# Kernel tuning notes

Hardware: AMD Instinct MI355X
Metric: run time of the kernel (lower is better)

The kernel has to match this reference:

```python
import jax, jax.numpy as jnp
import numpy as np
from jax.scipy.special import gammaln, xlogy

H, K, V = 8, 64, 192          # heads, key_size, value_size
F = 192                        # num_relative_position_features
LN2 = 0.6931471805599453


def positional_features(T):
    """Enformer positional basis: exp half-life, central mask, gamma pdf;
    non-symmetric -> concat [emb, sign(pos)*emb]. Returns [2T-1, F]."""
    n = F // 6                                  # basis per class per symmetry
    pos = jnp.arange(-(T - 1), T, dtype=jnp.float32)   # [2T-1]
    ap = jnp.abs(pos)[:, None]                  # [2T-1, 1]
    # exponential (min_half_life=3.0, seq_length=T)
    max_range = jnp.log(float(T)) / LN2
    half_life = 2.0 ** jnp.linspace(3.0, max_range, n)
    fe = jnp.exp(-LN2 / half_life * ap)
    # central mask
    widths = 2.0 ** jnp.arange(1, n + 1, dtype=jnp.float32) - 1.0
    fm = (widths > ap).astype(jnp.float32)
    # gamma (stddev=T/(2n), start_mean=T/n)
    stddev = T / (2.0 * n)
    mean = jnp.linspace(T / float(n), float(T), n)
    conc = (mean / stddev) ** 2
    rate = mean / stddev ** 2
    log_p = xlogy(conc - 1.0, ap) - rate * ap - (gammaln(conc) - conc * jnp.log(rate))
    prob = jnp.exp(log_p) + 1e-8
    fg = prob / jnp.max(prob)
    emb = jnp.concatenate([fe, fm, fg], axis=-1)               # [2T-1, F/2]
    emb = jnp.concatenate([emb, jnp.sign(pos)[:, None] * emb], axis=-1)  # [2T-1, F]
    return emb


def relative_shift(x):
    """TransformerXL relative shift. x: [B,H,T,2T-1] -> [B,H,T,T]."""
    b, h, t1, r = x.shape                       # r == 2*t1 - 1
    x = jnp.pad(x, ((0, 0), (0, 0), (0, 0), (1, 0)))  # [B,H,T,2T]
    x = x.reshape(b, h, r + 1, t1)[:, :, 1:, :]        # [B,H,2T-1,T]
    x = x.reshape(b, h, t1, r)
    return x[..., :t1]


def setup_inputs() -> dict:
    key = jax.random.key(0)
    ks = jax.random.split(key, 8)
    B, T, D = 2, 1536, 1536
    s = 0.02
    return {
        "x": jax.random.normal(ks[0], (B, T, D), jnp.float32),
        "Wq": jax.random.normal(ks[1], (D, H * K), jnp.float32) * s,
        "Wk": jax.random.normal(ks[2], (D, H * K), jnp.float32) * s,
        "Wv": jax.random.normal(ks[3], (D, H * V), jnp.float32) * s,
        "Wrk": jax.random.normal(ks[4], (F, H * K), jnp.float32) * s,
        "Wemb": jax.random.normal(ks[5], (H * V, D), jnp.float32) * s,
        "r_w_bias": jax.random.normal(ks[6], (1, H, 1, K), jnp.float32) * s,
        "r_r_bias": jax.random.normal(ks[7], (1, H, 1, K), jnp.float32) * s,
    }


def reference(x, Wq, Wk, Wv, Wrk, Wemb, r_w_bias, r_r_bias):
    B, T, D = x.shape
    q = (x @ Wq).reshape(B, T, H, K).transpose(0, 2, 1, 3)   # [B,H,T,K]
    k = (x @ Wk).reshape(B, T, H, K).transpose(0, 2, 1, 3)
    v = (x @ Wv).reshape(B, T, H, V).transpose(0, 2, 1, 3)   # [B,H,T,V]
    q = q * (K ** -0.5)                                       # scaling
    emb = positional_features(T)                              # [2T-1, F]
    r_k = (emb @ Wrk).reshape(2 * T - 1, H, K).transpose(1, 0, 2)  # [H,2T-1,K]
    content = jnp.einsum('bhqk,bhmk->bhqm', q + r_w_bias, k)       # [B,H,T,T]
    rel = jnp.einsum('bhqk,hmk->bhqm', q + r_r_bias, r_k)          # [B,H,T,2T-1]
    logits = content + relative_shift(rel)
    w = jax.nn.softmax(logits, axis=-1)
    out = jnp.einsum('bhqm,bhmv->bhqv', w, v)                      # [B,H,T,V]
    out = out.transpose(0, 2, 1, 3).reshape(B, T, H * V)
    return out @ Wemb
```

## Files before the change

kernel.cpp:

```cpp
#include <hip/hip_runtime.h>
#include <stdint.h>

#define DEVI __device__ __forceinline__
#define LOG2E 1.4426950408889634f

typedef short bf16x8 __attribute__((ext_vector_type(8)));
typedef float f32x4 __attribute__((ext_vector_type(4)));

#define PMAX 0.01867013f

DEVI float b2f(unsigned short u) {
  union { unsigned u32; float f; } x;
  x.u32 = ((unsigned)u) << 16;
  return x.f;
}
DEVI unsigned short f2b(float f) {
  union { float f32; unsigned u32; } x;
  x.f32 = f;
  unsigned u = x.u32;
  return (unsigned short)((u + 0x7FFFu + ((u >> 16) & 1u)) >> 16);
}

DEVI void gload16(const unsigned short* g, unsigned short* l) {
  __builtin_amdgcn_global_load_lds(
      (const __attribute__((address_space(1))) void*)g,
      (__attribute__((address_space(3))) void*)l, 16, 0, 0);
}

DEVI float gamma_prob(float ap, int i) {
  float mean = 48.f * (float)(i + 1);
  float conc = (mean / 24.f) * (mean / 24.f);
  float rate = mean / 576.f;
  if (ap == 0.f) return 1e-8f;
  float logp = (conc - 1.f) * logf(ap) - rate * ap - (lgammaf(conc) - conc * logf(rate));
  return expf(logp) + 1e-8f;
}

DEVI void dev_transpose(const float* srcf, const unsigned short* srcb, int src_ld,
                        unsigned short* dst, int dst_ld, int rows, int cols,
                        int bx, int by, unsigned short (*t)[33]) {
  int tx = threadIdx.x & 31, ty = threadIdx.x >> 5;
  int r0 = by * 32, c0 = bx * 32;
#pragma unroll
  for (int i = 0; i < 4; i++) {
    int r = r0 + ty + i * 8, cc = c0 + tx;
    if (r < rows && cc < cols)
      t[ty + i * 8][tx] = srcf ? f2b(srcf[(size_t)r * src_ld + cc])
                               : srcb[(size_t)r * src_ld + cc];
  }
  __syncthreads();
#pragma unroll
  for (int i = 0; i < 4; i++) {
    int dr = c0 + ty + i * 8, dc = r0 + tx;
    if (dr < cols && dc < rows) dst[(size_t)dr * dst_ld + dc] = t[tx][ty + i * 8];
  }
}

__global__ __launch_bounds__(256) void k_prep(
    const float* __restrict__ x, const float* __restrict__ Wq,
    const float* __restrict__ Wk, const float* __restrict__ Wv,
    const float* __restrict__ Wemb, const float* __restrict__ Wrk,
    unsigned short* __restrict__ xb, unsigned short* __restrict__ WqkvT,
    unsigned short* __restrict__ WembT, unsigned short* __restrict__ WrkT,
    unsigned short* __restrict__ emb) {
  __shared__ unsigned short t[32][33];
  int bid = blockIdx.x;
  if (bid < 4608) {
    int i = (bid * 256 + threadIdx.x) * 4;
    float4 v = *(const float4*)(x + i);
    ushort4 o;
    o.x = f2b(v.x); o.y = f2b(v.y); o.z = f2b(v.z); o.w = f2b(v.w);
    *(ushort4*)(xb + i) = o;
  } else if (bid < 5376) {
    int s = bid - 4608;
    dev_transpose(Wq, nullptr, 512, WqkvT, 1536, 1536, 512, s % 16, s / 16, t);
  } else if (bid < 6144) {
    int s = bid - 5376;
    dev_transpose(Wk, nullptr, 512, WqkvT + (size_t)512 * 1536, 1536, 1536, 512, s % 16, s / 16, t);
  } else if (bid < 8448) {
    int s = bid - 6144;
    dev_transpose(Wv, nullptr, 1536, WqkvT + (size_t)1024 * 1536, 1536, 1536, 1536, s % 48, s / 48, t);
  } else if (bid < 10752) {
    int s = bid - 8448;
    dev_transpose(Wemb, nullptr, 1536, WembT, 1536, 1536, 1536, s % 48, s / 48, t);
  } else if (bid < 10848) {
    int s = bid - 10752;
    dev_transpose(Wrk, nullptr, 512, WrkT, 192, 192, 512, s % 16, s / 16, t);
  } else {
    int idx = (bid - 10848) * 256 + threadIdx.x;
    if (idx < 3071 * 96) {
      int m = idx / 96, cc = idx % 96;
      float ap = fabsf((float)(m - 1535));
      float val;
      if (cc < 32) {
        float max_range = logf(1536.f) * 1.4426950408889634f;
        float l = 3.f + (float)cc * (max_range - 3.f) / 31.f;
        val = exp2f(-ap * exp2f(-l));
      } else if (cc < 64) {
        float width = exp2f((float)(cc - 31)) - 1.f;
        val = (width > ap) ? 1.f : 0.f;
      } else {
        val = gamma_prob(ap, cc - 64) / PMAX;
      }
      float sgn = (m > 1535) ? 1.f : ((m < 1535) ? -1.f : 0.f);
      emb[(size_t)m * 192 + cc] = f2b(val);
      emb[(size_t)m * 192 + 96 + cc] = f2b(sgn * val);
    }
  }
}

DEVI void dev_gemm(const unsigned short* __restrict__ A, const unsigned short* __restrict__ Bt,
                   unsigned short* Cb, float* Cf, int M, int N, int K,
                   int bx, int by, unsigned short* As, unsigned short* Bs) {
  int tid = threadIdx.x;
  int w = tid >> 6, L = tid & 63, g = L >> 4, c = L & 15;
  int m0 = by << 7, n0 = bx << 7;
  int wm = (w >> 1) << 6, wn = (w & 1) << 6;
  f32x4 acc[4][4];
#pragma unroll
  for (int i = 0; i < 4; i++)
#pragma unroll
    for (int j = 0; j < 4; j++) acc[i][j] = (f32x4){0.f, 0.f, 0.f, 0.f};
  int nkt = K >> 5;
  for (int kt = 0; kt < nkt; kt++) {
    int k0 = kt << 5;
#pragma unroll
    for (int i2 = 0; i2 < 2; i2++) {
      int cidx = tid + (i2 << 8);
      int row = cidx >> 2, kc = (cidx & 3) << 3;
      int ra = m0 + row;
      if (ra >= M) ra = M - 1;
      gload16(A + (size_t)ra * K + k0 + kc, As + cidx * 8);
      gload16(Bt + (size_t)(n0 + row) * K + k0 + kc, Bs + cidx * 8);
    }
    __syncthreads();
    bf16x8 af[4], bfr[4];
#pragma unroll
    for (int t = 0; t < 4; t++) af[t] = *(const bf16x8*)(As + (wm + t * 16 + c) * 32 + g * 8);
#pragma unroll
    for (int t = 0; t < 4; t++) bfr[t] = *(const bf16x8*)(Bs + (wn + t * 16 + c) * 32 + g * 8);
#pragma unroll
    for (int mt = 0; mt < 4; mt++)
#pragma unroll
      for (int nt = 0; nt < 4; nt++)
        acc[mt][nt] = __builtin_amdgcn_mfma_f32_16x16x32_bf16(af[mt], bfr[nt], acc[mt][nt], 0, 0, 0);
    __syncthreads();
  }
#pragma unroll
  for (int mt = 0; mt < 4; mt++)
#pragma unroll
    for (int nt = 0; nt < 4; nt++)
#pragma unroll
      for (int r = 0; r < 4; r++) {
        int rr = m0 + wm + mt * 16 + g * 4 + r;
        if (rr < M) {
          size_t o = (size_t)rr * N + n0 + wn + nt * 16 + c;
          if (Cf) Cf[o] = acc[mt][nt][r];
          else Cb[o] = f2b(acc[mt][nt][r]);
        }
      }
}

__global__ __launch_bounds__(256) void k_gemm(
    const unsigned short* __restrict__ A, const unsigned short* __restrict__ Bt,
    unsigned short* Cb, float* Cf, int M, int N, int K) {
  __shared__ unsigned short sm[8192];
  dev_gemm(A, Bt, Cb, Cf, M, N, K, blockIdx.x, blockIdx.y, sm, sm + 4096);
}

__global__ __launch_bounds__(256) void k_mid(
    const unsigned short* __restrict__ emb, const unsigned short* __restrict__ WrkT,
    unsigned short* __restrict__ rkb, const unsigned short* __restrict__ QKV,
    unsigned short* __restrict__ Vt) {
  __shared__ unsigned short sm[8192];
  int bid = blockIdx.x;
  if (bid < 96) {
    dev_gemm(emb, WrkT, rkb, nullptr, 3071, 512, 192, bid & 3, bid >> 2, sm, sm + 4096);
  } else {
    int tt = bid - 96;
    int which = tt / 2304;
    tt %= 2304;
    dev_transpose(nullptr, QKV + 1024 + (size_t)which * 1536 * 2560, 2560,
                  Vt + (size_t)which * 1536 * 1536, 1536, 1536, 1536,
                  tt % 48, tt / 48, (unsigned short (*)[33])sm);
  }
}

__global__ __launch_bounds__(256, 2) void k_attn(
    const unsigned short* __restrict__ QKV, const unsigned short* __restrict__ rk,
    const unsigned short* __restrict__ Vt, const float* __restrict__ rwb,
    const float* __restrict__ rrb, unsigned short* __restrict__ Opart,
    float* __restrict__ lpart) {
  __shared__ unsigned short lds[24576];
  const int tid = threadIdx.x;
  const int w = tid >> 6, L = tid & 63, g = L >> 4, c = L & 15;
  const int bid = blockIdx.x;
  const int h = bid & 7, b = (bid >> 3) & 1, kh = (bid >> 4) & 3;
  const int i0b = (bid >> 6) << 7;
  const int qp = i0b + w * 32;
  const int bh = b * 8 + h;
  const int c7s = (c & 7) << 3;

  const int lrow8 = L >> 3;
  const int lbo = (((L & 7) * 16) ^ ((lrow8 & 7) << 4));

  bf16x8 aqw[2][2], aqr[2][2];
#pragma unroll
  for (int qi = 0; qi < 2; qi++) {
    const unsigned short* qrow =
        QKV + (size_t)(b * 1536 + qp + qi * 16 + c) * 2560 + h * 64;
#pragma unroll
    for (int ks = 0; ks < 2; ks++) {
      union { bf16x8 v; unsigned short s[8]; } uw, ur;
#pragma unroll
      for (int j = 0; j < 8; j++) {
        int d = ks * 32 + g * 8 + j;
        float qv = b2f(qrow[d]) * 0.125f;
        uw.s[j] = f2b((qv + rwb[h * 64 + d]) * LOG2E);
        ur.s[j] = f2b((qv + rrb[h * 64 + d]) * LOG2E);
      }
      aqw[qi][ks] = uw.v;
      aqr[qi][ks] = ur.v;
    }
  }

  int baddr[4], bsel[4];
#pragma unroll
  for (int r = 0; r < 4; r++) {
    int u = c - (g * 4 + r) + 15;
    baddr[r] = (((g << 4) | (u & 15)) << 2);
    bsel[r] = (u >> 4) & 1;
  }

  f32x4 Ofr[8][3];
#pragma unroll
  for (int s = 0; s < 8; s++)
#pragma unroll
    for (int t = 0; t < 3; t++) Ofr[s][t] = (f32x4){0.f, 0.f, 0.f, 0.f};
  float lrow[2][4] = {{0.f, 0.f, 0.f, 0.f}, {0.f, 0.f, 0.f, 0.f}};

  const unsigned short* rkh = rk + h * 64;
  const size_t kgbase = (size_t)(b * 1536 + kh * 384) * 2560 + 512 + h * 64;
  const size_t vgbase = (size_t)(bh * 192) * 1536 + kh * 384;

  auto stageK = [&](int kt) {
#pragma unroll
    for (int i = 0; i < 2; i++) {
      int key = w * 16 + i * 8 + lrow8;
      const unsigned short* src =
          QKV + kgbase + (size_t)(kt * 64 + key) * 2560 + (lbo >> 1);
      gload16(src, lds + w * 1024 + i * 512);
    }
  };
  auto stageV = [&](int kt) {
#pragma unroll
    for (int i = 0; i < 6; i++) {
      int vd = w * 48 + i * 8 + lrow8;
      const unsigned short* src =
          Vt + vgbase + (size_t)vd * 1536 + kt * 64 + (lbo >> 1);
      gload16(src, lds + 4096 + w * 3072 + i * 512);
    }
  };

  stageK(0);
  __syncthreads();

  for (int jt = 0; jt < 6; jt++) {
    stageV(jt);

    const int j0g = kh * 384 + jt * 64;
    const int moff1 = j0g - (qp + 16) + 1520;

    f32x4 Sc[2][4];
#pragma unroll
    for (int nt = 0; nt < 4; nt++) {
      const int kro = (nt * 16 + c) * 64;
      bf16x8 kf0 = *(const bf16x8*)(lds + kro + ((g * 8) ^ c7s));
      bf16x8 kf1 = *(const bf16x8*)(lds + kro + ((32 + g * 8) ^ c7s));
      f32x4 z0 = (f32x4){0.f, 0.f, 0.f, 0.f};
      z0 = __builtin_amdgcn_mfma_f32_16x16x32_bf16(aqw[0][0], kf0, z0, 0, 0, 0);
      z0 = __builtin_amdgcn_mfma_f32_16x16x32_bf16(aqw[0][1], kf1, z0, 0, 0, 0);
      Sc[0][nt] = z0;
      f32x4 z1 = (f32x4){0.f, 0.f, 0.f, 0.f};
      z1 = __builtin_amdgcn_mfma_f32_16x16x32_bf16(aqw[1][0], kf0, z1, 0, 0, 0);
      z1 = __builtin_amdgcn_mfma_f32_16x16x32_bf16(aqw[1][1], kf1, z1, 0, 0, 0);
      Sc[1][nt] = z1;
    }

    float bandp0[4], bandp1[4];
    {
      int mg = moff1 + c;
      const unsigned short* rrow = rkh + (size_t)mg * 512;
      f32x4 z = (f32x4){0.f, 0.f, 0.f, 0.f};
      z = __builtin_amdgcn_mfma_f32_16x16x32_bf16(aqr[1][0], *(const bf16x8*)(rrow + g * 8), z, 0, 0, 0);
      z = __builtin_amdgcn_mfma_f32_16x16x32_bf16(aqr[1][1], *(const bf16x8*)(rrow + 32 + g * 8), z, 0, 0, 0);
#pragma unroll
      for (int r = 0; r < 4; r++)
        bandp1[r] = __int_as_float(__builtin_amdgcn_ds_bpermute(baddr[r], __float_as_int(z[r])));
    }
#pragma unroll
    for (int j = 1; j <= 5; j++) {
      int mg = moff1 + 16 * j + c;
      if (mg > 3070) mg = 3070;
      const unsigned short* rrow = rkh + (size_t)mg * 512;
      bf16x8 rf0 = *(const bf16x8*)(rrow + g * 8);
      bf16x8 rf1 = *(const bf16x8*)(rrow + 32 + g * 8);
      {
        f32x4 z = (f32x4){0.f, 0.f, 0.f, 0.f};
        z = __builtin_amdgcn_mfma_f32_16x16x32_bf16(aqr[0][0], rf0, z, 0, 0, 0);
        z = __builtin_amdgcn_mfma_f32_16x16x32_bf16(aqr[0][1], rf1, z, 0, 0, 0);
        if (j == 1) {
#pragma unroll
          for (int r = 0; r < 4; r++)
            bandp0[r] = __int_as_float(__builtin_amdgcn_ds_bpermute(baddr[r], __float_as_int(z[r])));
        } else {
          const int nt = j - 2;
#pragma unroll
          for (int r = 0; r < 4; r++) {
            float bandc = __int_as_float(__builtin_amdgcn_ds_bpermute(baddr[r], __float_as_int(z[r])));
            Sc[0][nt][r] += bsel[r] ? bandc : bandp0[r];
            bandp0[r] = bandc;
          }
        }
      }
      if (j <= 4) {
        f32x4 z = (f32x4){0.f, 0.f, 0.f, 0.f};
        z = __builtin_amdgcn_mfma_f32_16x16x32_bf16(aqr[1][0], rf0, z, 0, 0, 0);
        z = __builtin_amdgcn_mfma_f32_16x16x32_bf16(aqr[1][1], rf1, z, 0, 0, 0);
        const int nt = j - 1;
#pragma unroll
        for (int r = 0; r < 4; r++) {
          float bandc = __int_as_float(__builtin_amdgcn_ds_bpermute(baddr[r], __float_as_int(z[r])));
          Sc[1][nt][r] += bsel[r] ? bandc : bandp1[r];
          bandp1[r] = bandc;
        }
      }
    }

#pragma unroll
    for (int qi = 0; qi < 2; qi++) {
      unsigned short* slab = lds + 16384 + (2 * w + qi) * 1024;
#pragma unroll
      for (int nt = 0; nt < 4; nt++)
#pragma unroll
        for (int r = 0; r < 4; r++) {
          float p = exp2f(Sc[qi][nt][r]);
          lrow[qi][r] += p;
          int q = g * 4 + r;
          slab[q * 64 + ((nt * 16 + c) ^ ((q & 7) << 3))] = f2b(p);
        }
    }

    __syncthreads();

    if (jt < 5) stageK(jt + 1);

    bf16x8 vf0[3], vf1[3];
#pragma unroll
    for (int vt = 0; vt < 3; vt++) {
      const int vro = 4096 + (w * 48 + vt * 16 + c) * 64;
      vf0[vt] = *(const bf16x8*)(lds + vro + ((g * 8) ^ c7s));
      vf1[vt] = *(const bf16x8*)(lds + vro + ((32 + g * 8) ^ c7s));
    }
    __builtin_amdgcn_s_setprio(1);
#pragma unroll
    for (int s = 0; s < 8; s++) {
      const unsigned short* slab = lds + 16384 + s * 1024;
      bf16x8 ap0 = *(const bf16x8*)(slab + c * 64 + ((g * 8) ^ c7s));
      bf16x8 ap1 = *(const bf16x8*)(slab + c * 64 + ((32 + g * 8) ^ c7s));
#pragma unroll
      for (int vt = 0; vt < 3; vt++) {
        Ofr[s][vt] = __builtin_amdgcn_mfma_f32_16x16x32_bf16(ap0, vf0[vt], Ofr[s][vt], 0, 0, 0);
        Ofr[s][vt] = __builtin_amdgcn_mfma_f32_16x16x32_bf16(ap1, vf1[vt], Ofr[s][vt], 0, 0, 0);
      }
    }
    __builtin_amdgcn_s_setprio(0);

    __syncthreads();
  }

#pragma unroll
  for (int qi = 0; qi < 2; qi++)
#pragma unroll
    for (int r = 0; r < 4; r++) {
      float s = lrow[qi][r];
      s += __shfl_xor(s, 1, 64);
      s += __shfl_xor(s, 2, 64);
      s += __shfl_xor(s, 4, 64);
      s += __shfl_xor(s, 8, 64);
      lrow[qi][r] = s;
    }
  if (c == 0) {
#pragma unroll
    for (int qi = 0; qi < 2; qi++)
#pragma unroll
      for (int r = 0; r < 4; r++)
        lpart[(size_t)((kh * 2 + b) * 8 + h) * 1536 + qp + qi * 16 + g * 4 + r] =
            lrow[qi][r];
  }
#pragma unroll
  for (int s = 0; s < 8; s++)
#pragma unroll
    for (int vt = 0; vt < 3; vt++)
#pragma unroll
      for (int r = 0; r < 4; r++)
        Opart[(size_t)(kh * 3072 + b * 1536 + i0b + s * 16 + g * 4 + r) * 1536 +
              h * 192 + w * 48 + vt * 16 + c] = f2b(Ofr[s][vt][r]);
}

__global__ __launch_bounds__(256) void k_fin(
    const unsigned short* __restrict__ Op, const float* __restrict__ lp,
    unsigned short* __restrict__ O) {
  int idx = (blockIdx.x * 256 + threadIdx.x) * 8;
  int row = idx / 1536, c0 = idx % 1536;
  int b = row >= 1536;
  int q = row - b * 1536, hh = c0 / 192;
  float l = 0.f;
#pragma unroll
  for (int kh = 0; kh < 4; kh++)
    l += lp[(size_t)((kh * 2 + b) * 8 + hh) * 1536 + q];
  float sc = 1.f / l;
  float acc[8] = {0.f, 0.f, 0.f, 0.f, 0.f, 0.f, 0.f, 0.f};
#pragma unroll
  for (int kh = 0; kh < 4; kh++) {
    const ushort4* p = (const ushort4*)(Op + (size_t)(kh * 3072 + row) * 1536 + c0);
#pragma unroll
    for (int half = 0; half < 2; half++) {
      ushort4 a = p[half];
      acc[half * 4 + 0] += b2f(a.x);
      acc[half * 4 + 1] += b2f(a.y);
      acc[half * 4 + 2] += b2f(a.z);
      acc[half * 4 + 3] += b2f(a.w);
    }
  }
#pragma unroll
  for (int half = 0; half < 2; half++) {
    ushort4 o;
    o.x = f2b(acc[half * 4 + 0] * sc);
    o.y = f2b(acc[half * 4 + 1] * sc);
    o.z = f2b(acc[half * 4 + 2] * sc);
    o.w = f2b(acc[half * 4 + 3] * sc);
    *(ushort4*)(O + (size_t)row * 1536 + c0 + half * 4) = o;
  }
}

extern "C" void kernel_launch(void* const* d_in, const int* in_sizes, int n_in,
                              void* d_out, int out_size, void* d_ws, size_t ws_size,
                              hipStream_t stream) {
  const float* x    = (const float*)d_in[0];
  const float* Wq   = (const float*)d_in[1];
  const float* Wk   = (const float*)d_in[2];
  const float* Wv   = (const float*)d_in[3];
  const float* Wrk  = (const float*)d_in[4];
  const float* Wemb = (const float*)d_in[5];
  const float* rwb  = (const float*)d_in[6];
  const float* rrb  = (const float*)d_in[7];

  char* ws = (char*)d_ws;
  size_t off = 0;
  auto alloc = [&](size_t bytes) -> void* {
    void* p = ws + off;
    off += (bytes + 255) & ~(size_t)255;
    return p;
  };
  unsigned short* xb    = (unsigned short*)alloc((size_t)3072 * 1536 * 2);
  unsigned short* WqkvT = (unsigned short*)alloc((size_t)2560 * 1536 * 2);
  unsigned short* WembT = (unsigned short*)alloc((size_t)1536 * 1536 * 2);
  unsigned short* WrkT  = (unsigned short*)alloc((size_t)512 * 192 * 2);
  unsigned short* QKV   = (unsigned short*)alloc((size_t)3072 * 2560 * 2);
  unsigned short* Vt    = (unsigned short*)alloc((size_t)2 * 1536 * 1536 * 2);
  unsigned short* emb   = (unsigned short*)alloc((size_t)3072 * 192 * 2);
  unsigned short* rkb   = (unsigned short*)alloc((size_t)3072 * 512 * 2);
  unsigned short* Obuf  = (unsigned short*)alloc((size_t)3072 * 1536 * 2);
  unsigned short* Opart = (unsigned short*)alloc((size_t)4 * 3072 * 1536 * 2);
  float*          lpart = (float*)alloc((size_t)4 * 2 * 8 * 1536 * 4);

  k_prep<<<12000, 256, 0, stream>>>(x, Wq, Wk, Wv, Wemb, Wrk, xb, WqkvT, WembT, WrkT, emb);
  k_gemm<<<dim3(20, 24), 256, 0, stream>>>(xb, WqkvT, QKV, nullptr, 3072, 2560, 1536);
  k_mid<<<4704, 256, 0, stream>>>(emb, WrkT, rkb, QKV, Vt);
  k_attn<<<768, 256, 0, stream>>>(QKV, rkb, Vt, rwb, rrb, Opart, lpart);
  k_fin<<<2304, 256, 0, stream>>>(Opart, lpart, Obuf);
  k_gemm<<<dim3(12, 24), 256, 0, stream>>>(Obuf, WembT, nullptr, (float*)d_out, 3072, 1536, 1536);
}
```

Before: 278.8 us.

## Fuse V transpose into QKV projection GEMM epilogue and merge projection launches

Splits the QKV projection so the V part is computed by a GEMM variant whose epilogue writes directly in transposed Vt layout, removing the separate transpose pass and the V columns of the QKV buffer. The Q/K GEMM, V GEMM and the r_k GEMM are merged into one launch, eliminating one kernel launch and the intermediate round trip through global memory. QKV stride shrinks to 1024 and the attention kernel is updated accordingly. The transposed epilogue writes 4-element column chunks strided across rows, which may be less coalesced than the original row-major stores.

```diff
diff --git a/kernel.cpp b/kernel.cpp
--- a/kernel.cpp
+++ b/kernel.cpp
@@ -161,6 +161,59 @@
       }
 }
 
+DEVI void dev_gemm_vt(const unsigned short* __restrict__ A, const unsigned short* __restrict__ Bt,
+                      unsigned short* __restrict__ Vt, int M, int N, int K,
+                      int bx, int by, unsigned short* As, unsigned short* Bs) {
+  int tid = threadIdx.x;
+  int w = tid >> 6, L = tid & 63, g = L >> 4, c = L & 15;
+  int m0 = by << 7, n0 = bx << 7;
+  int wm = (w >> 1) << 6, wn = (w & 1) << 6;
+  f32x4 acc[4][4];
+#pragma unroll
+  for (int i = 0; i < 4; i++)
+#pragma unroll
+    for (int j = 0; j < 4; j++) acc[i][j] = (f32x4){0.f, 0.f, 0.f, 0.f};
+  int nkt = K >> 5;
+  for (int kt = 0; kt < nkt; kt++) {
+    int k0 = kt << 5;
+#pragma unroll
+    for (int i2 = 0; i2 < 2; i2++) {
+      int cidx = tid + (i2 << 8);
+      int row = cidx >> 2, kc = (cidx & 3) << 3;
+      gload16(A + (size_t)(m0 + row) * K + k0 + kc, As + cidx * 8);
+      gload16(Bt + (size_t)(n0 + row) * K + k0 + kc, Bs + cidx * 8);
+    }
+    __syncthreads();
+    bf16x8 af[4], bfr[4];
+#pragma unroll
+    for (int t = 0; t < 4; t++) af[t] = *(const bf16x8*)(As + (wm + t * 16 + c) * 32 + g * 8);
+#pragma unroll
+    for (int t = 0; t < 4; t++) bfr[t] = *(const bf16x8*)(Bs + (wn + t * 16 + c) * 32 + g * 8);
+#pragma unroll
+    for (int mt = 0; mt < 4; mt++)
+#pragma unroll
+      for (int nt = 0; nt < 4; nt++)
+        acc[mt][nt] = __builtin_amdgcn_mfma_f32_16x16x32_bf16(af[mt], bfr[nt], acc[mt][nt], 0, 0, 0);
+    __syncthreads();
+  }
+#pragma unroll
+  for (int mt = 0; mt < 4; mt++) {
+    int rr = m0 + wm + mt * 16 + g * 4;
+    int bb = rr >= 1536;
+    int tok = rr - bb * 1536;
+#pragma unroll
+    for (int nt = 0; nt < 4; nt++) {
+      int cc = n0 + wn + nt * 16 + c;
+      ushort4 o;
+      o.x = f2b(acc[mt][nt][0]);
+      o.y = f2b(acc[mt][nt][1]);
+      o.z = f2b(acc[mt][nt][2]);
+      o.w = f2b(acc[mt][nt][3]);
+      *(ushort4*)(Vt + (size_t)(bb * 1536 + cc) * 1536 + tok) = o;
+    }
+  }
+}
+
 __global__ __launch_bounds__(256) void k_gemm(
     const unsigned short* __restrict__ A, const unsigned short* __restrict__ Bt,
     unsigned short* Cb, float* Cf, int M, int N, int K) {
@@ -168,21 +221,22 @@
   dev_gemm(A, Bt, Cb, Cf, M, N, K, blockIdx.x, blockIdx.y, sm, sm + 4096);
 }
 
-__global__ __launch_bounds__(256) void k_mid(
+__global__ __launch_bounds__(256) void k_proj(
+    const unsigned short* __restrict__ xb, const unsigned short* __restrict__ WqkvT,
+    unsigned short* __restrict__ QKV, unsigned short* __restrict__ Vt,
     const unsigned short* __restrict__ emb, const unsigned short* __restrict__ WrkT,
-    unsigned short* __restrict__ rkb, const unsigned short* __restrict__ QKV,
-    unsigned short* __restrict__ Vt) {
+    unsigned short* __restrict__ rkb) {
   __shared__ unsigned short sm[8192];
   int bid = blockIdx.x;
-  if (bid < 96) {
-    dev_gemm(emb, WrkT, rkb, nullptr, 3071, 512, 192, bid & 3, bid >> 2, sm, sm + 4096);
+  if (bid < 288) {
+    dev_gemm_vt(xb, WqkvT + (size_t)1024 * 1536, Vt, 3072, 1536, 1536,
+                bid % 12, bid / 12, sm, sm + 4096);
+  } else if (bid < 480) {
+    int s = bid - 288;
+    dev_gemm(xb, WqkvT, QKV, nullptr, 3072, 1024, 1536, s % 8, s / 8, sm, sm + 4096);
   } else {
-    int tt = bid - 96;
-    int which = tt / 2304;
-    tt %= 2304;
-    dev_transpose(nullptr, QKV + 1024 + (size_t)which * 1536 * 2560, 2560,
-                  Vt + (size_t)which * 1536 * 1536, 1536, 1536, 1536,
-                  tt % 48, tt / 48, (unsigned short (*)[33])sm);
+    int s = bid - 480;
+    dev_gemm(emb, WrkT, rkb, nullptr, 3071, 512, 192, s & 3, s >> 2, sm, sm + 4096);
   }
 }
 
@@ -208,7 +262,7 @@
 #pragma unroll
   for (int qi = 0; qi < 2; qi++) {
     const unsigned short* qrow =
-        QKV + (size_t)(b * 1536 + qp + qi * 16 + c) * 2560 + h * 64;
+        QKV + (size_t)(b * 1536 + qp + qi * 16 + c) * 1024 + h * 64;
 #pragma unroll
     for (int ks = 0; ks < 2; ks++) {
       union { bf16x8 v; unsigned short s[8]; } uw, ur;
@@ -240,7 +294,7 @@
   float lrow[2][4] = {{0.f, 0.f, 0.f, 0.f}, {0.f, 0.f, 0.f, 0.f}};
 
   const unsigned short* rkh = rk + h * 64;
-  const size_t kgbase = (size_t)(b * 1536 + kh * 384) * 2560 + 512 + h * 64;
+  const size_t kgbase = (size_t)(b * 1536 + kh * 384) * 1024 + 512 + h * 64;
   const size_t vgbase = (size_t)(bh * 192) * 1536 + kh * 384;
 
   auto stageK = [&](int kt) {
@@ -248,7 +302,7 @@
     for (int i = 0; i < 2; i++) {
       int key = w * 16 + i * 8 + lrow8;
       const unsigned short* src =
-          QKV + kgbase + (size_t)(kt * 64 + key) * 2560 + (lbo >> 1);
+          QKV + kgbase + (size_t)(kt * 64 + key) * 1024 + (lbo >> 1);
       gload16(src, lds + w * 1024 + i * 512);
     }
   };
@@ -467,7 +521,7 @@
   unsigned short* WqkvT = (unsigned short*)alloc((size_t)2560 * 1536 * 2);
   unsigned short* WembT = (unsigned short*)alloc((size_t)1536 * 1536 * 2);
   unsigned short* WrkT  = (unsigned short*)alloc((size_t)512 * 192 * 2);
-  unsigned short* QKV   = (unsigned short*)alloc((size_t)3072 * 2560 * 2);
+  unsigned short* QKV   = (unsigned short*)alloc((size_t)3072 * 1024 * 2);
   unsigned short* Vt    = (unsigned short*)alloc((size_t)2 * 1536 * 1536 * 2);
   unsigned short* emb   = (unsigned short*)alloc((size_t)3072 * 192 * 2);
   unsigned short* rkb   = (unsigned short*)alloc((size_t)3072 * 512 * 2);
@@ -476,8 +530,7 @@
   float*          lpart = (float*)alloc((size_t)4 * 2 * 8 * 1536 * 4);
 
   k_prep<<<12000, 256, 0, stream>>>(x, Wq, Wk, Wv, Wemb, Wrk, xb, WqkvT, WembT, WrkT, emb);
-  k_gemm<<<dim3(20, 24), 256, 0, stream>>>(xb, WqkvT, QKV, nullptr, 3072, 2560, 1536);
-  k_mid<<<4704, 256, 0, stream>>>(emb, WrkT, rkb, QKV, Vt);
+  k_proj<<<576, 256, 0, stream>>>(xb, WqkvT, QKV, Vt, emb, WrkT, rkb);
   k_attn<<<768, 256, 0, stream>>>(QKV, rkb, Vt, rwb, rrb, Opart, lpart);
   k_fin<<<2304, 256, 0, stream>>>(Opart, lpart, Obuf);
   k_gemm<<<dim3(12, 24), 256, 0, stream>>>(Obuf, WembT, nullptr, (float*)d_out, 3072, 1536, 1536);
```

After: 258.2 us. 7.4% less time.
